# Performance work log

Hardware: AMD Instinct MI355X
Metric: run time of the kernel (lower is better)

Reference implementation:

```python
import jax, jax.numpy as jnp
import numpy as np

B, N, D = 4096, 128, 256


def setup_inputs() -> dict:
    key = jax.random.key(0)
    ks = jax.random.split(key, 6)
    return {
        "label": jax.random.normal(ks[0], (B, N, D), dtype=jnp.float32),
        "adj_in": jax.random.uniform(ks[1], (N, N), dtype=jnp.float32),
        "adj_out": jax.random.uniform(ks[2], (N, N), dtype=jnp.float32),
        "edge_bias": jnp.zeros((N, D), dtype=jnp.float32),
        "gate_weight": jax.random.normal(ks[3], (D, 1), dtype=jnp.float32) * (6.0 / (D + 1)) ** 0.5,
        "bias_gate": jnp.zeros((N, 1), dtype=jnp.float32),
        "out_edge_bias": jnp.zeros((N, D), dtype=jnp.float32),
        "out_gate_weight": jax.random.normal(ks[4], (D, 1), dtype=jnp.float32) * (6.0 / (D + 1)) ** 0.5,
        "out_bias_gate": jnp.zeros((N, 1), dtype=jnp.float32),
        "loop_gate": jax.random.normal(ks[5], (D, 1), dtype=jnp.float32) * (6.0 / (D + 1)) ** 0.5,
    }


def reference(label, adj_in, adj_out, edge_bias, gate_weight, bias_gate,
              out_edge_bias, out_gate_weight, out_bias_gate, loop_gate):
    h = label  # [B, N, D]
    # origin_adj is a constant buffer in the original module (detached numpy)
    origin = jax.lax.stop_gradient(jnp.where(adj_in <= 0, adj_in, 1.0))

    # in-arc branch: masked dense adjacency matmul + bias + scalar gate
    h_in = jnp.einsum('mn,bnd->bmd', origin * adj_in, h)            # [B, N, D]
    in_gate = jnp.einsum('bnd,do->bno', h, gate_weight) + bias_gate  # [B, N, 1]
    msg_in = (h_in + edge_bias) * jax.nn.sigmoid(in_gate)

    # out-arc branch: transposed mask times out adjacency
    h_out = jnp.einsum('mn,bnd->bmd', origin.T * adj_out, h)
    out_gate = jnp.einsum('bnd,do->bno', h, out_gate_weight) + out_bias_gate
    msg_out = (h_out + out_edge_bias) * jax.nn.sigmoid(out_gate)

    # self-loop branch
    lp_gate = jnp.einsum('bnd,do->bno', h, loop_gate)
    msg_loop = h * jax.nn.sigmoid(lp_gate)

    # dropout p=0.0 -> identity
    return jax.nn.relu(msg_in + msg_out + msg_loop)
```

## Files before the change

### kernel.cpp

```cpp
#include <hip/hip_runtime.h>
#include <hip/hip_bf16.h>

#define NN 128
#define ND 256

typedef __attribute__((ext_vector_type(8))) short short8v;
typedef __attribute__((ext_vector_type(4))) short short4v;
typedef __attribute__((ext_vector_type(4))) float floatx4;

__device__ __forceinline__ unsigned short f2bf(float x){
  unsigned u = __float_as_uint(x);
  u += 0x7FFF + ((u >> 16) & 1);
  return (unsigned short)(u >> 16);
}

__global__ void prep_A(const float* __restrict__ adj_in, const float* __restrict__ adj_out,
                       unsigned short* __restrict__ Abf){
  int idx = blockIdx.x * 256 + threadIdx.x;
  int m = idx >> 7, n = idx & 127;
  float v;
  if (m < NN){
    float a = adj_in[m * NN + n];
    v = (a <= 0.f) ? a * a : a;
  } else {
    int mm = m - NN;
    float t = adj_in[n * NN + mm];
    float o = (t <= 0.f) ? t : 1.f;
    v = o * adj_out[mm * NN + n];
  }
  Abf[idx] = f2bf(v);
}

__global__ __launch_bounds__(512, 4) void gcn_main(
    const float* __restrict__ H, const unsigned short* __restrict__ Abf,
    const float* __restrict__ eb,  const float* __restrict__ gw,
    const float* __restrict__ bg,  const float* __restrict__ oeb,
    const float* __restrict__ ogw, const float* __restrict__ obg,
    const float* __restrict__ lw,  float* __restrict__ Out)
{
  __shared__ __align__(16) unsigned short Ht[ND * NN];
  __shared__ float sigS[3 * NN];

  const int tid  = threadIdx.x;
  const int wave = tid >> 6;
  const int lane = tid & 63;
  const int g    = lane >> 4;
  const int m16  = lane & 15;
  const int b    = blockIdx.x;
  const float* Hb = H   + (size_t)b * NN * ND;
  float*       Ob = Out + (size_t)b * NN * ND;

  const int G  = 4 * wave + g;
  const int n0 = 4 * G;
  float sacc[12];
  #pragma unroll
  for (int i = 0; i < 12; ++i) sacc[i] = 0.f;

  #pragma unroll
  for (int dq = 0; dq < 4; ++dq){
    const int d0 = 64 * dq + 4 * m16;
    const floatx4 wa = *(const floatx4*)(gw  + d0);
    const floatx4 wb = *(const floatx4*)(ogw + d0);
    const floatx4 wc = *(const floatx4*)(lw  + d0);
    floatx4 rr[4];
    #pragma unroll
    for (int ro = 0; ro < 4; ++ro)
      rr[ro] = *(const floatx4*)(Hb + (size_t)(n0 + ro) * ND + d0);
    #pragma unroll
    for (int ro = 0; ro < 4; ++ro){
      const floatx4 r = rr[ro];
      sacc[3*ro+0] += r[0]*wa[0] + r[1]*wa[1] + r[2]*wa[2] + r[3]*wa[3];
      sacc[3*ro+1] += r[0]*wb[0] + r[1]*wb[1] + r[2]*wb[2] + r[3]*wb[3];
      sacc[3*ro+2] += r[0]*wc[0] + r[1]*wc[1] + r[2]*wc[2] + r[3]*wc[3];
    }
    #pragma unroll
    for (int j = 0; j < 4; ++j){
      const int d = d0 + j;
      short4v pv;
      pv[0] = (short)f2bf(rr[0][j]);
      pv[1] = (short)f2bf(rr[1][j]);
      pv[2] = (short)f2bf(rr[2][j]);
      pv[3] = (short)f2bf(rr[3][j]);
      *(short4v*)&Ht[d * NN + (n0 ^ (((d >> 1) & 7) << 3))] = pv;
    }
  }
  #pragma unroll
  for (int m = 1; m < 16; m <<= 1){
    #pragma unroll
    for (int i = 0; i < 12; ++i) sacc[i] += __shfl_xor(sacc[i], m, 64);
  }
  if (m16 == 0){
    #pragma unroll
    for (int ro = 0; ro < 4; ++ro){
      const int n = n0 + ro;
      sigS[n]          = 1.f / (1.f + __expf(-(sacc[3*ro+0] + bg[n])));
      sigS[NN + n]     = 1.f / (1.f + __expf(-(sacc[3*ro+1] + obg[n])));
      sigS[2*NN + n]   = 1.f / (1.f + __expf(-sacc[3*ro+2]));
    }
  }
  __syncthreads();

  const int mrow = 16 * wave + m16;
  const float si = sigS[mrow];
  const float so = sigS[NN + mrow];
  const float sl = sigS[2 * NN + mrow];

  const floatx4 zz = {0.f, 0.f, 0.f, 0.f};
  #pragma unroll
  for (int pass = 0; pass < 2; ++pass){
    const int dbase = 128 * pass;
    floatx4 acc1[8], acc2[8];
    #pragma unroll
    for (int i = 0; i < 8; ++i){ acc1[i] = zz; acc2[i] = zz; }

    #pragma unroll
    for (int k0 = 0; k0 < 128; k0 += 32){
      const int kk = k0 + 8 * g;
      const short8v av1 = *(const short8v*)&Abf[ mrow        * 128 + kk];
      const short8v av2 = *(const short8v*)&Abf[(128 + mrow) * 128 + kk];
      #pragma unroll
      for (int df = 0; df < 8; ++df){
        const int d = dbase + 16 * df + m16;
        const short8v hv = *(const short8v*)&Ht[d * NN + (kk ^ (((d >> 1) & 7) << 3))];
        acc1[df] = __builtin_amdgcn_mfma_f32_16x16x32_bf16(hv, av1, acc1[df], 0, 0, 0);
        acc2[df] = __builtin_amdgcn_mfma_f32_16x16x32_bf16(hv, av2, acc2[df], 0, 0, 0);
      }
    }

    #pragma unroll
    for (int df = 0; df < 8; ++df){
      const int dcol = dbase + 16 * df + 4 * g;
      const floatx4 ebv  = *(const floatx4*)(eb  + mrow * ND + dcol);
      const floatx4 oebv = *(const floatx4*)(oeb + mrow * ND + dcol);
      const floatx4 hv4  = *(const floatx4*)(Hb  + (size_t)mrow * ND + dcol);
      floatx4 o;
      #pragma unroll
      for (int r = 0; r < 4; ++r){
        const float v = (acc1[df][r] + ebv[r]) * si
                      + (acc2[df][r] + oebv[r]) * so
                      + hv4[r] * sl;
        o[r] = fmaxf(v, 0.f);
      }
      __builtin_nontemporal_store(o, (floatx4*)(Ob + (size_t)mrow * ND + dcol));
    }
  }
}

extern "C" void kernel_launch(void* const* d_in, const int* in_sizes, int n_in,
                              void* d_out, int out_size, void* d_ws, size_t ws_size,
                              hipStream_t stream){
  const float* H    = (const float*)d_in[0];
  const float* ain  = (const float*)d_in[1];
  const float* aout = (const float*)d_in[2];
  const float* eb   = (const float*)d_in[3];
  const float* gwp  = (const float*)d_in[4];
  const float* bgp  = (const float*)d_in[5];
  const float* oebp = (const float*)d_in[6];
  const float* ogwp = (const float*)d_in[7];
  const float* obgp = (const float*)d_in[8];
  const float* lwp  = (const float*)d_in[9];
  unsigned short* Abf = (unsigned short*)d_ws;

  prep_A<<<128, 256, 0, stream>>>(ain, aout, Abf);
  gcn_main<<<4096, 512, 0, stream>>>(H, Abf, eb, gwp, bgp, oebp, ogwp, obgp, lwp,
                                     (float*)d_out);
}
```

Before: 446.2 us.

## Compute gate projections with MFMA and reuse LDS bf16 H for self-loop

Packs the three gate weight vectors into a bf16 MFMA operand during the prep kernel and computes all three per-row gate logits with one MFMA chain per wave, replacing scalar dot products and cross-lane shuffle reductions. The epilogue now reads the self-loop input from the bf16 transposed tile in shared memory instead of re-reading fp32 H from global memory. This cuts VALU work and global traffic but lowers the gate and self-loop inputs to bf16 precision. It also adds strided LDS reads in the epilogue.

```diff
diff --git a/kernel.cpp b/kernel.cpp
--- a/kernel.cpp
+++ b/kernel.cpp
@@ -13,30 +13,41 @@
   u += 0x7FFF + ((u >> 16) & 1);
   return (unsigned short)(u >> 16);
 }
+__device__ __forceinline__ float bf2f(unsigned short h){
+  return __uint_as_float(((unsigned)h) << 16);
+}
 
 __global__ void prep_A(const float* __restrict__ adj_in, const float* __restrict__ adj_out,
-                       unsigned short* __restrict__ Abf){
+                       const float* __restrict__ gw, const float* __restrict__ ogw,
+                       const float* __restrict__ lw, unsigned short* __restrict__ Abf){
   int idx = blockIdx.x * 256 + threadIdx.x;
-  int m = idx >> 7, n = idx & 127;
-  float v;
-  if (m < NN){
-    float a = adj_in[m * NN + n];
-    v = (a <= 0.f) ? a * a : a;
-  } else {
-    int mm = m - NN;
-    float t = adj_in[n * NN + mm];
-    float o = (t <= 0.f) ? t : 1.f;
-    v = o * adj_out[mm * NN + n];
+  if (idx < 32768){
+    int m = idx >> 7, n = idx & 127;
+    float v;
+    if (m < NN){
+      float a = adj_in[m * NN + n];
+      v = (a <= 0.f) ? a * a : a;
+    } else {
+      int mm = m - NN;
+      float t = adj_in[n * NN + mm];
+      float o = (t <= 0.f) ? t : 1.f;
+      v = o * adj_out[mm * NN + n];
+    }
+    Abf[idx] = f2bf(v);
+  } else if (idx < 32768 + 4096){
+    int t   = idx - 32768;
+    int j   = t & 7, m16 = (t >> 3) & 15, g = (t >> 7) & 3, kc = t >> 9;
+    int d   = kc * 32 + 8 * g + j;
+    float v = (m16 == 0) ? gw[d] : (m16 == 1) ? ogw[d] : (m16 == 2) ? lw[d] : 0.f;
+    Abf[idx] = f2bf(v);
   }
-  Abf[idx] = f2bf(v);
 }
 
 __global__ __launch_bounds__(512, 4) void gcn_main(
     const float* __restrict__ H, const unsigned short* __restrict__ Abf,
-    const float* __restrict__ eb,  const float* __restrict__ gw,
-    const float* __restrict__ bg,  const float* __restrict__ oeb,
-    const float* __restrict__ ogw, const float* __restrict__ obg,
-    const float* __restrict__ lw,  float* __restrict__ Out)
+    const float* __restrict__ eb,  const float* __restrict__ bg,
+    const float* __restrict__ oeb, const float* __restrict__ obg,
+    float* __restrict__ Out)
 {
   __shared__ __align__(16) unsigned short Ht[ND * NN];
   __shared__ float sigS[3 * NN];
@@ -49,30 +60,33 @@
   const int b    = blockIdx.x;
   const float* Hb = H   + (size_t)b * NN * ND;
   float*       Ob = Out + (size_t)b * NN * ND;
+  const unsigned short* WgT = Abf + 32768;
 
-  const int G  = 4 * wave + g;
-  const int n0 = 4 * G;
-  float sacc[12];
+  const int G    = 4 * wave + g;
+  const int n0   = 4 * G;
+  const int arow = 16 * wave + m16;
+
+  floatx4 gacc = {0.f, 0.f, 0.f, 0.f};
   #pragma unroll
-  for (int i = 0; i < 12; ++i) sacc[i] = 0.f;
-
-  #pragma unroll
-  for (int dq = 0; dq < 4; ++dq){
-    const int d0 = 64 * dq + 4 * m16;
-    const floatx4 wa = *(const floatx4*)(gw  + d0);
-    const floatx4 wb = *(const floatx4*)(ogw + d0);
-    const floatx4 wc = *(const floatx4*)(lw  + d0);
+  for (int s = 0; s < 4; ++s){
+    #pragma unroll
+    for (int t = 0; t < 2; ++t){
+      const int k0 = 64 * s + 32 * t;
+      const floatx4 f0 = *(const floatx4*)(Hb + (size_t)arow * ND + k0 + 8 * g);
+      const floatx4 f1 = *(const floatx4*)(Hb + (size_t)arow * ND + k0 + 8 * g + 4);
+      const short8v wv = *(const short8v*)&WgT[(((k0 >> 5) * 4 + g) * 16 + m16) * 8];
+      short8v af;
+      af[0] = (short)f2bf(f0[0]); af[1] = (short)f2bf(f0[1]);
+      af[2] = (short)f2bf(f0[2]); af[3] = (short)f2bf(f0[3]);
+      af[4] = (short)f2bf(f1[0]); af[5] = (short)f2bf(f1[1]);
+      af[6] = (short)f2bf(f1[2]); af[7] = (short)f2bf(f1[3]);
+      gacc = __builtin_amdgcn_mfma_f32_16x16x32_bf16(af, wv, gacc, 0, 0, 0);
+    }
+    const int d0 = 64 * s + 4 * m16;
     floatx4 rr[4];
     #pragma unroll
     for (int ro = 0; ro < 4; ++ro)
       rr[ro] = *(const floatx4*)(Hb + (size_t)(n0 + ro) * ND + d0);
-    #pragma unroll
-    for (int ro = 0; ro < 4; ++ro){
-      const floatx4 r = rr[ro];
-      sacc[3*ro+0] += r[0]*wa[0] + r[1]*wa[1] + r[2]*wa[2] + r[3]*wa[3];
-      sacc[3*ro+1] += r[0]*wb[0] + r[1]*wb[1] + r[2]*wb[2] + r[3]*wb[3];
-      sacc[3*ro+2] += r[0]*wc[0] + r[1]*wc[1] + r[2]*wc[2] + r[3]*wc[3];
-    }
     #pragma unroll
     for (int j = 0; j < 4; ++j){
       const int d = d0 + j;
@@ -84,26 +98,21 @@
       *(short4v*)&Ht[d * NN + (n0 ^ (((d >> 1) & 7) << 3))] = pv;
     }
   }
-  #pragma unroll
-  for (int m = 1; m < 16; m <<= 1){
+  if (m16 < 3){
     #pragma unroll
-    for (int i = 0; i < 12; ++i) sacc[i] += __shfl_xor(sacc[i], m, 64);
-  }
-  if (m16 == 0){
-    #pragma unroll
-    for (int ro = 0; ro < 4; ++ro){
-      const int n = n0 + ro;
-      sigS[n]          = 1.f / (1.f + __expf(-(sacc[3*ro+0] + bg[n])));
-      sigS[NN + n]     = 1.f / (1.f + __expf(-(sacc[3*ro+1] + obg[n])));
-      sigS[2*NN + n]   = 1.f / (1.f + __expf(-sacc[3*ro+2]));
+    for (int r = 0; r < 4; ++r){
+      const int n = 16 * wave + 4 * g + r;
+      float x = gacc[r];
+      if (m16 == 0)      x += bg[n];
+      else if (m16 == 1) x += obg[n];
+      sigS[m16 * NN + n] = 1.f / (1.f + __expf(-x));
     }
   }
   __syncthreads();
 
-  const int mrow = 16 * wave + m16;
-  const float si = sigS[mrow];
-  const float so = sigS[NN + mrow];
-  const float sl = sigS[2 * NN + mrow];
+  const float si = sigS[arow];
+  const float so = sigS[NN + arow];
+  const float sl = sigS[2 * NN + arow];
 
   const floatx4 zz = {0.f, 0.f, 0.f, 0.f};
   #pragma unroll
@@ -116,8 +125,8 @@
     #pragma unroll
     for (int k0 = 0; k0 < 128; k0 += 32){
       const int kk = k0 + 8 * g;
-      const short8v av1 = *(const short8v*)&Abf[ mrow        * 128 + kk];
-      const short8v av2 = *(const short8v*)&Abf[(128 + mrow) * 128 + kk];
+      const short8v av1 = *(const short8v*)&Abf[ arow        * 128 + kk];
+      const short8v av2 = *(const short8v*)&Abf[(128 + arow) * 128 + kk];
       #pragma unroll
       for (int df = 0; df < 8; ++df){
         const int d = dbase + 16 * df + m16;
@@ -130,18 +139,23 @@
     #pragma unroll
     for (int df = 0; df < 8; ++df){
       const int dcol = dbase + 16 * df + 4 * g;
-      const floatx4 ebv  = *(const floatx4*)(eb  + mrow * ND + dcol);
-      const floatx4 oebv = *(const floatx4*)(oeb + mrow * ND + dcol);
-      const floatx4 hv4  = *(const floatx4*)(Hb  + (size_t)mrow * ND + dcol);
+      const floatx4 ebv  = *(const floatx4*)(eb  + arow * ND + dcol);
+      const floatx4 oebv = *(const floatx4*)(oeb + arow * ND + dcol);
+      float hl[4];
+      #pragma unroll
+      for (int r = 0; r < 4; ++r){
+        const int d = dcol + r;
+        hl[r] = bf2f(Ht[d * NN + (arow ^ (((d >> 1) & 7) << 3))]);
+      }
       floatx4 o;
       #pragma unroll
       for (int r = 0; r < 4; ++r){
         const float v = (acc1[df][r] + ebv[r]) * si
                       + (acc2[df][r] + oebv[r]) * so
-                      + hv4[r] * sl;
+                      + hl[r] * sl;
         o[r] = fmaxf(v, 0.f);
       }
-      __builtin_nontemporal_store(o, (floatx4*)(Ob + (size_t)mrow * ND + dcol));
+      __builtin_nontemporal_store(o, (floatx4*)(Ob + (size_t)arow * ND + dcol));
     }
   }
 }
@@ -161,7 +175,6 @@
   const float* lwp  = (const float*)d_in[9];
   unsigned short* Abf = (unsigned short*)d_ws;
 
-  prep_A<<<128, 256, 0, stream>>>(ain, aout, Abf);
-  gcn_main<<<4096, 512, 0, stream>>>(H, Abf, eb, gwp, bgp, oebp, ogwp, obgp, lwp,
-                                     (float*)d_out);
+  prep_A<<<144, 256, 0, stream>>>(ain, aout, gwp, ogwp, lwp, Abf);
+  gcn_main<<<4096, 512, 0, stream>>>(H, Abf, eb, bgp, oebp, obgp, (float*)d_out);
 }
```

Result: faster. 373.8 us (-16.2%).
